# Kernel optimization log

Hardware: AMD Instinct MI355X
Metric: run time of the kernel (lower is better)

## Reference

```python
import math
import jax, jax.numpy as jnp
import numpy as np

N_HEADS = 8

def setup_inputs() -> dict:
    key = jax.random.key(0)
    qkv = jax.random.normal(key, (4, 3 * N_HEADS * 64, 2048), dtype=jnp.float32)
    return {"qkv": qkv}

def reference(qkv) -> jnp.ndarray:
    bs, width, length = qkv.shape
    assert width % (3 * N_HEADS) == 0
    ch = width // (3 * N_HEADS)
    q, k, v = jnp.split(qkv, 3, axis=1)            # each [N, H*C, T]
    scale = 1.0 / math.sqrt(math.sqrt(ch))
    qh = (q * scale).reshape(bs * N_HEADS, ch, length)  # [BH, C, T]
    kh = (k * scale).reshape(bs * N_HEADS, ch, length)
    vh = v.reshape(bs * N_HEADS, ch, length)
    weight = jnp.einsum('bct,bcs->bts', qh, kh)    # [BH, T, T]
    weight = jax.nn.softmax(weight.astype(jnp.float32), axis=-1).astype(weight.dtype)
    a = jnp.einsum('bts,bcs->bct', weight, vh)     # [BH, C, T]
    return a.reshape(bs, -1, length)
```

## Files before the change

### kernel.cpp

```cpp
#include <hip/hip_runtime.h>

#define T_LEN 2048
#define CH 64
#define NH 8
#define STILE 64
#define TTILE 256
#define WT 32
#define NIT (T_LEN / STILE)
#define KSZ (STILE * CH)
#define CS 72
#define QS 260
#define RS 68

#define QSCALE 0.180336880972948929f

typedef __attribute__((ext_vector_type(4))) float  f32x4;
typedef __attribute__((ext_vector_type(8))) __bf16 bf16x8;
typedef __attribute__((ext_vector_type(4))) __bf16 bf16x4;
typedef __attribute__((ext_vector_type(2))) __bf16 bf16x2;
typedef __attribute__((ext_vector_type(2))) unsigned int uint2v;
typedef __attribute__((ext_vector_type(4))) unsigned int uint4v;

union SMem {
  float qstage[CH * QS];
  struct {
    __bf16 k_hi[2][KSZ];
    __bf16 v_s [2][CH * CS];
  } loop;
  struct {
    float o[8][WT][RS];
    float l[2][8][4][16];
  } red;
};

#define MFMA(A, B, C) __builtin_amdgcn_mfma_f32_16x16x32_bf16((A), (B), (C), 0, 0, 0)

__device__ __forceinline__ unsigned pkbf2(float lo, float hi) {
  bf16x2 t = {(__bf16)lo, (__bf16)hi};
  return __builtin_bit_cast(unsigned, t);
}

__device__ __forceinline__ void load_k8(const float* kp, int s0, int stid, float (&kr)[8]) {
  int s  = stid & 63;
  int cg = stid >> 6;
  const float* kc = kp + (size_t)(8 * cg) * T_LEN + s0 + s;
#pragma unroll
  for (int j = 0; j < 8; ++j)
    kr[j] = kc[(size_t)j * T_LEN];
}

__device__ __forceinline__ void store_k8(__bf16* kh, int stid, const float (&kr)[8]) {
  int s  = stid & 63;
  int cg = stid >> 6;
  uint4v wv = {pkbf2(kr[0], kr[1]), pkbf2(kr[2], kr[3]),
               pkbf2(kr[4], kr[5]), pkbf2(kr[6], kr[7])};
  bf16x8 w = __builtin_bit_cast(bf16x8, wv);
  int e = (s << 6) + (cg << 3);
  *(bf16x8*)&kh[e ^ ((s & 7) << 3)] = w;
}

__device__ __forceinline__ void load_v(const float* vp, int s0, int ltid, f32x4 (&vreg)[2]) {
  int c  = ltid >> 3;
  int s8 = (ltid & 7) << 3;
  const float* vc = vp + (size_t)c * T_LEN + s0 + s8;
  vreg[0] = *(const f32x4*)(vc);
  vreg[1] = *(const f32x4*)(vc + 4);
}

__device__ __forceinline__ void store_v(__bf16* vs, int ltid, const f32x4 (&vreg)[2]) {
  int c  = ltid >> 3;
  int s8 = (ltid & 7) << 3;
  uint4v wv = {pkbf2(vreg[0].x, vreg[0].y), pkbf2(vreg[0].z, vreg[0].w),
               pkbf2(vreg[1].x, vreg[1].y), pkbf2(vreg[1].z, vreg[1].w)};
  *(bf16x8*)&vs[c * CS + s8] = __builtin_bit_cast(bf16x8, wv);
}

__global__ __launch_bounds__(1024, 4)
void qkv_attn_mfma(const float* __restrict__ qkv, float* __restrict__ out) {
  __shared__ SMem sm;
  const int tid  = threadIdx.x;
  const int lane = tid & 63;
  const int wave = tid >> 6;
  const int wt   = wave & 7;
  const int ws   = wave >> 3;
  const int tn   = lane & 15;
  const int quad = lane >> 4;
  const int stid = tid & 511;

  const int d0 = blockIdx.x;
  const int w  = ((d0 & 7) << 5) | (d0 >> 3);
  const int ttile = w & 7;
  const int bh    = w >> 3;
  const int b = bh >> 3, h = bh & 7;
  const size_t base = (size_t)b * (3 * NH * CH) * T_LEN;
  const float* qp = qkv + base + (size_t)(CH * h) * T_LEN;
  const float* kp = qkv + base + (size_t)(CH * (NH + h)) * T_LEN;
  const float* vp = qkv + base + (size_t)(CH * (2 * NH + h)) * T_LEN;
  const int t0 = ttile * TTILE;

#pragma unroll
  for (int rr = 0; rr < 4; ++rr) {
    int fidx = rr * 1024 + tid;
    int c  = fidx >> 6;
    int t4 = (fidx & 63) << 2;
    f32x4 q4 = *(const f32x4*)(qp + (size_t)c * T_LEN + t0 + t4);
    *(f32x4*)&sm.qstage[c * QS + t4] = q4;
  }
  __syncthreads();

  bf16x8 qh[2][2];
#pragma unroll
  for (int nb = 0; nb < 2; ++nb)
#pragma unroll
    for (int kb = 0; kb < 2; ++kb) {
      int tloc = wt * WT + nb * 16 + tn;
      bf16x8 H;
#pragma unroll
      for (int j = 0; j < 8; ++j) {
        float qv = sm.qstage[(kb * 32 + quad * 8 + j) * QS + tloc] * QSCALE;
        H[j] = (__bf16)qv;
      }
      qh[nb][kb] = H;
    }
  __syncthreads();

  f32x4 acc[4][2];
  f32x4 acc_l[2];
#pragma unroll
  for (int mbc = 0; mbc < 4; ++mbc)
#pragma unroll
    for (int nb = 0; nb < 2; ++nb)
      acc[mbc][nb] = (f32x4){0.f, 0.f, 0.f, 0.f};
  acc_l[0] = (f32x4){0.f, 0.f, 0.f, 0.f};
  acc_l[1] = (f32x4){0.f, 0.f, 0.f, 0.f};

  bf16x8 av_one;
#pragma unroll
  for (int j = 0; j < 8; ++j) av_one[j] = (__bf16)1.0f;

  float  kreg[8];
  f32x4  vreg[2];
  if (ws == 0) { load_k8(kp, 0, stid, kreg); store_k8(sm.loop.k_hi[0], stid, kreg); }
  else         { load_v (vp, 0, stid, vreg); store_v (sm.loop.v_s[0], stid, vreg); }
  __syncthreads();

  for (int it = 0; it < NIT; ++it) {
    const int cur = it & 1;
    const bool more = (it + 1 < NIT);

    if (more) {
      if (ws == 0) load_k8(kp, (it + 1) * STILE, stid, kreg);
      else         load_v (vp, (it + 1) * STILE, stid, vreg);
    }

    const __bf16* kh = sm.loop.k_hi[cur];
    const int swz = (tn & 7) << 3;
    bf16x8 ah[2][2];
#pragma unroll
    for (int mb = 0; mb < 2; ++mb) {
      const int srow = 32 * ws + 16 * mb + tn;
#pragma unroll
      for (int kb = 0; kb < 2; ++kb) {
        int e = (srow << 6) + 32 * kb + 8 * quad;
        ah[mb][kb] = *(const bf16x8*)&kh[e ^ swz];
      }
    }
    __builtin_amdgcn_s_setprio(1);
    f32x4 d[2][2];
#pragma unroll
    for (int mb = 0; mb < 2; ++mb)
#pragma unroll
      for (int nb = 0; nb < 2; ++nb) {
        f32x4 t = (f32x4){0.f, 0.f, 0.f, 0.f};
        t = MFMA(ah[mb][0], qh[nb][0], t);
        t = MFMA(ah[mb][1], qh[nb][1], t);
        d[mb][nb] = t;
      }
    __builtin_amdgcn_s_setprio(0);

    const __bf16* vs = sm.loop.v_s[cur];
    bf16x8 av[4];
#pragma unroll
    for (int mbc = 0; mbc < 4; ++mbc)
      av[mbc] = *(const bf16x8*)&vs[(16 * mbc + tn) * CS + 32 * ws + quad * 8];

    bf16x8 bp[2];
#pragma unroll
    for (int nb = 0; nb < 2; ++nb) {
#pragma unroll
      for (int mb = 0; mb < 2; ++mb)
#pragma unroll
        for (int r = 0; r < 4; ++r)
          d[mb][nb][r] = __builtin_amdgcn_exp2f(d[mb][nb][r]);
      unsigned u00 = pkbf2(d[0][nb][0], d[0][nb][1]);
      unsigned u01 = pkbf2(d[0][nb][2], d[0][nb][3]);
      unsigned u10 = pkbf2(d[1][nb][0], d[1][nb][1]);
      unsigned u11 = pkbf2(d[1][nb][2], d[1][nb][3]);
      uint2v s0 = __builtin_amdgcn_permlane32_swap(u00, u10, false, false);
      uint2v r0 = __builtin_amdgcn_permlane16_swap(s0.x, s0.y, false, false);
      uint2v s1 = __builtin_amdgcn_permlane32_swap(u01, u11, false, false);
      uint2v r1 = __builtin_amdgcn_permlane16_swap(s1.x, s1.y, false, false);
      uint4v wv = {r0.x, r1.x, r0.y, r1.y};
      bp[nb] = __builtin_bit_cast(bf16x8, wv);
    }

    __builtin_amdgcn_s_setprio(1);
#pragma unroll
    for (int mbc = 0; mbc < 4; ++mbc)
#pragma unroll
      for (int nb = 0; nb < 2; ++nb)
        acc[mbc][nb] = MFMA(av[mbc], bp[nb], acc[mbc][nb]);
#pragma unroll
    for (int nb = 0; nb < 2; ++nb)
      acc_l[nb] = MFMA(av_one, bp[nb], acc_l[nb]);
    __builtin_amdgcn_s_setprio(0);

    if (more) {
      if (ws == 0) store_k8(sm.loop.k_hi[cur ^ 1], stid, kreg);
      else         store_v (sm.loop.v_s [cur ^ 1], stid, vreg);
    }
    __syncthreads();
  }

  float l_part[2] = {acc_l[0][0], acc_l[1][0]};

  if (ws == 1) {
#pragma unroll
    for (int nb = 0; nb < 2; ++nb) {
      sm.red.l[nb][wt][quad][tn] = l_part[nb];
#pragma unroll
      for (int mbc = 0; mbc < 4; ++mbc)
        *(f32x4*)&sm.red.o[wt][nb * 16 + tn][16 * mbc + quad * 4] = acc[mbc][nb];
    }
  }
  __syncthreads();
  if (ws == 0) {
    float* op = out + (size_t)bh * CH * T_LEN;
#pragma unroll
    for (int nb = 0; nb < 2; ++nb) {
      float l = l_part[nb] + sm.red.l[nb][wt][quad][tn];
      float inv_l = 1.0f / l;
      int t = t0 + wt * WT + nb * 16 + tn;
#pragma unroll
      for (int mbc = 0; mbc < 4; ++mbc) {
        f32x4 o = acc[mbc][nb] + *(const f32x4*)&sm.red.o[wt][nb * 16 + tn][16 * mbc + quad * 4];
        o = o * inv_l;
        int c = 16 * mbc + quad * 4;
        op[(size_t)(c + 0) * T_LEN + t] = o.x;
        op[(size_t)(c + 1) * T_LEN + t] = o.y;
        op[(size_t)(c + 2) * T_LEN + t] = o.z;
        op[(size_t)(c + 3) * T_LEN + t] = o.w;
      }
    }
  }
}

extern "C" void kernel_launch(void* const* d_in, const int* in_sizes, int n_in,
                              void* d_out, int out_size, void* d_ws, size_t ws_size,
                              hipStream_t stream) {
  const float* qkv = (const float*)d_in[0];
  float* out = (float*)d_out;
  dim3 grid(256);
  qkv_attn_mfma<<<grid, 1024, 0, stream>>>(qkv, out);
}
```

Baseline: 118.5 us.

## Use 512-thread blocks with each wave covering full S tile, drop cross-wave reduction

Halves the block to 8 waves. Each wave now processes both 32-column halves of every S tile, where before two wave groups split the S dimension and merged partial O and l sums through shared memory. This removes the final LDS reduction and its barrier, and lets each thread load both K and V. The cost is half as many waves per block to hide latency, and each wave does twice the serial MFMA work per iteration.

```diff
diff --git a/kernel.cpp b/kernel.cpp
--- a/kernel.cpp
+++ b/kernel.cpp
@@ -10,7 +10,6 @@
 #define KSZ (STILE * CH)
 #define CS 72
 #define QS 260
-#define RS 68
 
 #define QSCALE 0.180336880972948929f
 
@@ -27,10 +26,6 @@
     __bf16 k_hi[2][KSZ];
     __bf16 v_s [2][CH * CS];
   } loop;
-  struct {
-    float o[8][WT][RS];
-    float l[2][8][4][16];
-  } red;
 };
 
 #define MFMA(A, B, C) __builtin_amdgcn_mfma_f32_16x16x32_bf16((A), (B), (C), 0, 0, 0)
@@ -40,18 +35,18 @@
   return __builtin_bit_cast(unsigned, t);
 }
 
-__device__ __forceinline__ void load_k8(const float* kp, int s0, int stid, float (&kr)[8]) {
-  int s  = stid & 63;
-  int cg = stid >> 6;
+__device__ __forceinline__ void load_k8(const float* kp, int s0, int tid, float (&kr)[8]) {
+  int s  = tid & 63;
+  int cg = tid >> 6;
   const float* kc = kp + (size_t)(8 * cg) * T_LEN + s0 + s;
 #pragma unroll
   for (int j = 0; j < 8; ++j)
     kr[j] = kc[(size_t)j * T_LEN];
 }
 
-__device__ __forceinline__ void store_k8(__bf16* kh, int stid, const float (&kr)[8]) {
-  int s  = stid & 63;
-  int cg = stid >> 6;
+__device__ __forceinline__ void store_k8(__bf16* kh, int tid, const float (&kr)[8]) {
+  int s  = tid & 63;
+  int cg = tid >> 6;
   uint4v wv = {pkbf2(kr[0], kr[1]), pkbf2(kr[2], kr[3]),
                pkbf2(kr[4], kr[5]), pkbf2(kr[6], kr[7])};
   bf16x8 w = __builtin_bit_cast(bf16x8, wv);
@@ -59,33 +54,30 @@
   *(bf16x8*)&kh[e ^ ((s & 7) << 3)] = w;
 }
 
-__device__ __forceinline__ void load_v(const float* vp, int s0, int ltid, f32x4 (&vreg)[2]) {
-  int c  = ltid >> 3;
-  int s8 = (ltid & 7) << 3;
+__device__ __forceinline__ void load_v(const float* vp, int s0, int tid, f32x4 (&vreg)[2]) {
+  int c  = tid >> 3;
+  int s8 = (tid & 7) << 3;
   const float* vc = vp + (size_t)c * T_LEN + s0 + s8;
   vreg[0] = *(const f32x4*)(vc);
   vreg[1] = *(const f32x4*)(vc + 4);
 }
 
-__device__ __forceinline__ void store_v(__bf16* vs, int ltid, const f32x4 (&vreg)[2]) {
-  int c  = ltid >> 3;
-  int s8 = (ltid & 7) << 3;
+__device__ __forceinline__ void store_v(__bf16* vs, int tid, const f32x4 (&vreg)[2]) {
+  int c  = tid >> 3;
+  int s8 = (tid & 7) << 3;
   uint4v wv = {pkbf2(vreg[0].x, vreg[0].y), pkbf2(vreg[0].z, vreg[0].w),
                pkbf2(vreg[1].x, vreg[1].y), pkbf2(vreg[1].z, vreg[1].w)};
   *(bf16x8*)&vs[c * CS + s8] = __builtin_bit_cast(bf16x8, wv);
 }
 
-__global__ __launch_bounds__(1024, 4)
+__global__ __launch_bounds__(512, 1)
 void qkv_attn_mfma(const float* __restrict__ qkv, float* __restrict__ out) {
   __shared__ SMem sm;
   const int tid  = threadIdx.x;
   const int lane = tid & 63;
-  const int wave = tid >> 6;
-  const int wt   = wave & 7;
-  const int ws   = wave >> 3;
+  const int wt   = tid >> 6;
   const int tn   = lane & 15;
   const int quad = lane >> 4;
-  const int stid = tid & 511;
 
   const int d0 = blockIdx.x;
   const int w  = ((d0 & 7) << 5) | (d0 >> 3);
@@ -99,8 +91,8 @@
   const int t0 = ttile * TTILE;
 
 #pragma unroll
-  for (int rr = 0; rr < 4; ++rr) {
-    int fidx = rr * 1024 + tid;
+  for (int rr = 0; rr < 8; ++rr) {
+    int fidx = rr * 512 + tid;
     int c  = fidx >> 6;
     int t4 = (fidx & 63) << 2;
     f32x4 q4 = *(const f32x4*)(qp + (size_t)c * T_LEN + t0 + t4);
@@ -140,8 +132,10 @@
 
   float  kreg[8];
   f32x4  vreg[2];
-  if (ws == 0) { load_k8(kp, 0, stid, kreg); store_k8(sm.loop.k_hi[0], stid, kreg); }
-  else         { load_v (vp, 0, stid, vreg); store_v (sm.loop.v_s[0], stid, vreg); }
+  load_k8(kp, 0, tid, kreg);
+  load_v (vp, 0, tid, vreg);
+  store_k8(sm.loop.k_hi[0], tid, kreg);
+  store_v (sm.loop.v_s[0], tid, vreg);
   __syncthreads();
 
   for (int it = 0; it < NIT; ++it) {
@@ -149,108 +143,98 @@
     const bool more = (it + 1 < NIT);
 
     if (more) {
-      if (ws == 0) load_k8(kp, (it + 1) * STILE, stid, kreg);
-      else         load_v (vp, (it + 1) * STILE, stid, vreg);
+      load_k8(kp, (it + 1) * STILE, tid, kreg);
+      load_v (vp, (it + 1) * STILE, tid, vreg);
     }
 
     const __bf16* kh = sm.loop.k_hi[cur];
+    const __bf16* vs = sm.loop.v_s[cur];
     const int swz = (tn & 7) << 3;
-    bf16x8 ah[2][2];
-#pragma unroll
-    for (int mb = 0; mb < 2; ++mb) {
-      const int srow = 32 * ws + 16 * mb + tn;
-#pragma unroll
-      for (int kb = 0; kb < 2; ++kb) {
-        int e = (srow << 6) + 32 * kb + 8 * quad;
-        ah[mb][kb] = *(const bf16x8*)&kh[e ^ swz];
+
+#pragma unroll
+    for (int hh = 0; hh < 2; ++hh) {
+      const int sbase = 32 * hh;
+
+      bf16x8 ah[2][2];
+#pragma unroll
+      for (int mb = 0; mb < 2; ++mb) {
+        const int srow = sbase + 16 * mb + tn;
+#pragma unroll
+        for (int kb = 0; kb < 2; ++kb) {
+          int e = (srow << 6) + 32 * kb + 8 * quad;
+          ah[mb][kb] = *(const bf16x8*)&kh[e ^ swz];
+        }
       }
-    }
-    __builtin_amdgcn_s_setprio(1);
-    f32x4 d[2][2];
-#pragma unroll
-    for (int mb = 0; mb < 2; ++mb)
+      __builtin_amdgcn_s_setprio(1);
+      f32x4 d[2][2];
+#pragma unroll
+      for (int mb = 0; mb < 2; ++mb)
+#pragma unroll
+        for (int nb = 0; nb < 2; ++nb) {
+          f32x4 t = (f32x4){0.f, 0.f, 0.f, 0.f};
+          t = MFMA(ah[mb][0], qh[nb][0], t);
+          t = MFMA(ah[mb][1], qh[nb][1], t);
+          d[mb][nb] = t;
+        }
+      __builtin_amdgcn_s_setprio(0);
+
+      bf16x8 av[4];
+#pragma unroll
+      for (int mbc = 0; mbc < 4; ++mbc)
+        av[mbc] = *(const bf16x8*)&vs[(16 * mbc + tn) * CS + sbase + quad * 8];
+
+      bf16x8 bp[2];
 #pragma unroll
       for (int nb = 0; nb < 2; ++nb) {
-        f32x4 t = (f32x4){0.f, 0.f, 0.f, 0.f};
-        t = MFMA(ah[mb][0], qh[nb][0], t);
-        t = MFMA(ah[mb][1], qh[nb][1], t);
-        d[mb][nb] = t;
+#pragma unroll
+        for (int mb = 0; mb < 2; ++mb)
+#pragma unroll
+          for (int r = 0; r < 4; ++r)
+            d[mb][nb][r] = __builtin_amdgcn_exp2f(d[mb][nb][r]);
+        unsigned u00 = pkbf2(d[0][nb][0], d[0][nb][1]);
+        unsigned u01 = pkbf2(d[0][nb][2], d[0][nb][3]);
+        unsigned u10 = pkbf2(d[1][nb][0], d[1][nb][1]);
+        unsigned u11 = pkbf2(d[1][nb][2], d[1][nb][3]);
+        uint2v s0 = __builtin_amdgcn_permlane32_swap(u00, u10, false, false);
+        uint2v r0 = __builtin_amdgcn_permlane16_swap(s0.x, s0.y, false, false);
+        uint2v s1 = __builtin_amdgcn_permlane32_swap(u01, u11, false, false);
+        uint2v r1 = __builtin_amdgcn_permlane16_swap(s1.x, s1.y, false, false);
+        uint4v wv = {r0.x, r1.x, r0.y, r1.y};
+        bp[nb] = __builtin_bit_cast(bf16x8, wv);
       }
-    __builtin_amdgcn_s_setprio(0);
-
-    const __bf16* vs = sm.loop.v_s[cur];
-    bf16x8 av[4];
-#pragma unroll
-    for (int mbc = 0; mbc < 4; ++mbc)
-      av[mbc] = *(const bf16x8*)&vs[(16 * mbc + tn) * CS + 32 * ws + quad * 8];
-
-    bf16x8 bp[2];
-#pragma unroll
-    for (int nb = 0; nb < 2; ++nb) {
-#pragma unroll
-      for (int mb = 0; mb < 2; ++mb)
-#pragma unroll
-        for (int r = 0; r < 4; ++r)
-          d[mb][nb][r] = __builtin_amdgcn_exp2f(d[mb][nb][r]);
-      unsigned u00 = pkbf2(d[0][nb][0], d[0][nb][1]);
-      unsigned u01 = pkbf2(d[0][nb][2], d[0][nb][3]);
-      unsigned u10 = pkbf2(d[1][nb][0], d[1][nb][1]);
-      unsigned u11 = pkbf2(d[1][nb][2], d[1][nb][3]);
-      uint2v s0 = __builtin_amdgcn_permlane32_swap(u00, u10, false, false);
-      uint2v r0 = __builtin_amdgcn_permlane16_swap(s0.x, s0.y, false, false);
-      uint2v s1 = __builtin_amdgcn_permlane32_swap(u01, u11, false, false);
-      uint2v r1 = __builtin_amdgcn_permlane16_swap(s1.x, s1.y, false, false);
-      uint4v wv = {r0.x, r1.x, r0.y, r1.y};
-      bp[nb] = __builtin_bit_cast(bf16x8, wv);
-    }
-
-    __builtin_amdgcn_s_setprio(1);
-#pragma unroll
-    for (int mbc = 0; mbc < 4; ++mbc)
+
+      __builtin_amdgcn_s_setprio(1);
+#pragma unroll
+      for (int mbc = 0; mbc < 4; ++mbc)
+#pragma unroll
+        for (int nb = 0; nb < 2; ++nb)
+          acc[mbc][nb] = MFMA(av[mbc], bp[nb], acc[mbc][nb]);
 #pragma unroll
       for (int nb = 0; nb < 2; ++nb)
-        acc[mbc][nb] = MFMA(av[mbc], bp[nb], acc[mbc][nb]);
-#pragma unroll
-    for (int nb = 0; nb < 2; ++nb)
-      acc_l[nb] = MFMA(av_one, bp[nb], acc_l[nb]);
-    __builtin_amdgcn_s_setprio(0);
+        acc_l[nb] = MFMA(av_one, bp[nb], acc_l[nb]);
+      __builtin_amdgcn_s_setprio(0);
+    }
 
     if (more) {
-      if (ws == 0) store_k8(sm.loop.k_hi[cur ^ 1], stid, kreg);
-      else         store_v (sm.loop.v_s [cur ^ 1], stid, vreg);
+      store_k8(sm.loop.k_hi[cur ^ 1], tid, kreg);
+      store_v (sm.loop.v_s [cur ^ 1], tid, vreg);
     }
     __syncthreads();
   }
 
-  float l_part[2] = {acc_l[0][0], acc_l[1][0]};
-
-  if (ws == 1) {
-#pragma unroll
-    for (int nb = 0; nb < 2; ++nb) {
-      sm.red.l[nb][wt][quad][tn] = l_part[nb];
-#pragma unroll
-      for (int mbc = 0; mbc < 4; ++mbc)
-        *(f32x4*)&sm.red.o[wt][nb * 16 + tn][16 * mbc + quad * 4] = acc[mbc][nb];
-    }
-  }
-  __syncthreads();
-  if (ws == 0) {
-    float* op = out + (size_t)bh * CH * T_LEN;
-#pragma unroll
-    for (int nb = 0; nb < 2; ++nb) {
-      float l = l_part[nb] + sm.red.l[nb][wt][quad][tn];
-      float inv_l = 1.0f / l;
-      int t = t0 + wt * WT + nb * 16 + tn;
-#pragma unroll
-      for (int mbc = 0; mbc < 4; ++mbc) {
-        f32x4 o = acc[mbc][nb] + *(const f32x4*)&sm.red.o[wt][nb * 16 + tn][16 * mbc + quad * 4];
-        o = o * inv_l;
-        int c = 16 * mbc + quad * 4;
-        op[(size_t)(c + 0) * T_LEN + t] = o.x;
-        op[(size_t)(c + 1) * T_LEN + t] = o.y;
-        op[(size_t)(c + 2) * T_LEN + t] = o.z;
-        op[(size_t)(c + 3) * T_LEN + t] = o.w;
-      }
+  float* op = out + (size_t)bh * CH * T_LEN;
+#pragma unroll
+  for (int nb = 0; nb < 2; ++nb) {
+    float inv_l = 1.0f / acc_l[nb][0];
+    int t = t0 + wt * WT + nb * 16 + tn;
+#pragma unroll
+    for (int mbc = 0; mbc < 4; ++mbc) {
+      f32x4 o = acc[mbc][nb] * inv_l;
+      int c = 16 * mbc + quad * 4;
+      op[(size_t)(c + 0) * T_LEN + t] = o.x;
+      op[(size_t)(c + 1) * T_LEN + t] = o.y;
+      op[(size_t)(c + 2) * T_LEN + t] = o.z;
+      op[(size_t)(c + 3) * T_LEN + t] = o.w;
     }
   }
 }
@@ -261,5 +245,5 @@
   const float* qkv = (const float*)d_in[0];
   float* out = (float*)d_out;
   dim3 grid(256);
-  qkv_attn_mfma<<<grid, 1024, 0, stream>>>(qkv, out);
-}
+  qkv_attn_mfma<<<grid, 512, 0, stream>>>(qkv, out);
+}
```

Result: slower. 121.8 us (+2.7%).
